# Performance work log

Measured on AMD Instinct MI355X. Metric: run time of the kernel, lower is better.

Reference implementation:

```python
import jax, jax.numpy as jnp
import numpy as np

THR = 1.0  # snntorch Leaky default threshold
BETA = 0.9


def setup_inputs() -> dict:
    key = jax.random.key(0)
    k_in, k_w1, k_b1, k_w2, k_b2 = jax.random.split(key, 5)
    T, B, D, H = 100, 256, 784, 256
    # binary spike train input (rate-coded)
    spike_input = (jax.random.uniform(k_in, (T, B, D)) < 0.5).astype(jnp.float32)
    # nn.Linear init: U(-1/sqrt(fan_in), 1/sqrt(fan_in))
    lim1 = 1.0 / np.sqrt(D)
    lim2 = 1.0 / np.sqrt(H)
    W1 = jax.random.uniform(k_w1, (H, D), minval=-lim1, maxval=lim1, dtype=jnp.float32)
    b1 = jax.random.uniform(k_b1, (H,), minval=-lim1, maxval=lim1, dtype=jnp.float32)
    W2 = jax.random.uniform(k_w2, (D, H), minval=-lim2, maxval=lim2, dtype=jnp.float32)
    b2 = jax.random.uniform(k_b2, (D,), minval=-lim2, maxval=lim2, dtype=jnp.float32)
    return {"spike_input": spike_input, "W1": W1, "b1": b1, "W2": W2, "b2": b2}


def _heaviside(x):
    return (x > 0).astype(x.dtype)


def reference(spike_input, W1, b1, W2, b2):
    T, B, D = spike_input.shape
    H = W1.shape[0]

    def step(carry, x_t):
        mem1, mem2 = carry
        # layer 1: Linear + Leaky LIF (reset-by-subtraction, as in snntorch)
        cur1 = x_t @ W1.T + b1                          # [B,H]
        reset1 = _heaviside(mem1 - THR)                 # spikes from previous mem
        mem1 = BETA * mem1 + cur1 - reset1 * THR
        spk1 = _heaviside(mem1 - THR)
        # layer 2
        cur2 = spk1 @ W2.T + b2                         # [B,D]
        reset2 = _heaviside(mem2 - THR)
        mem2 = BETA * mem2 + cur2 - reset2 * THR
        spk2 = _heaviside(mem2 - THR)
        return (mem1, mem2), spk2

    mem1_0 = jnp.zeros((B, H), dtype=spike_input.dtype)
    mem2_0 = jnp.zeros((B, D), dtype=spike_input.dtype)
    _, spk_out = jax.lax.scan(step, (mem1_0, mem2_0), spike_input)
    return spk_out  # [T,B,D]
```

## Files before the change

### kernel.cpp

```cpp
#include <hip/hip_runtime.h>

typedef __attribute__((ext_vector_type(8))) _Float16 f16x8;
typedef __attribute__((ext_vector_type(4))) float f32x4;

static constexpr int TT = 100, BB = 256, DD = 784, HH = 256;
static constexpr int MM = TT * BB;
static constexpr int K1PAD = 800;
static constexpr int DPAD = 832;
static constexpr float MIDSC = 2048.0f, INVMID = 1.0f / 2048.0f;

__device__ __forceinline__ unsigned short f2h(float x) {
  _Float16 h = (_Float16)x;
  return *(unsigned short*)&h;
}
__device__ __forceinline__ float h2f(unsigned short u) {
  _Float16 h = *(_Float16*)&u;
  return (float)h;
}
__device__ __forceinline__ void glds16(const void* g, void* l) {
  __builtin_amdgcn_global_load_lds(
      (const __attribute__((address_space(1))) unsigned int*)g,
      (__attribute__((address_space(3))) unsigned int*)l, 16, 0, 0);
}

__global__ __launch_bounds__(256)
void split_w(const float* __restrict__ W, unsigned short* __restrict__ Ws,
             int N, int K, int Npad, int Kpad) {
  int idx = blockIdx.x * 256 + threadIdx.x;
  int total = Npad * Kpad;
  if (idx >= total) return;
  int row = idx / Kpad, col = idx - row * Kpad;
  float w = (row < N && col < K) ? W[row * K + col] : 0.0f;
  unsigned short h0 = f2h(w);
  float r = (w - h2f(h0)) * MIDSC;
  Ws[idx] = h0;
  Ws[total + idx] = f2h(r);
}

__global__ __launch_bounds__(256, 2)
void gemm1(const float* __restrict__ X, const unsigned short* __restrict__ Bs,
           const float* __restrict__ bias, float* __restrict__ C) {
  constexpr int Kpad = K1PAD, nkb = Kpad / 32;
  __shared__ unsigned short Asm[2][128 * 32];
  __shared__ unsigned short Bsm[3][2][128 * 32];
  const int tid = threadIdx.x;
  const int bm = blockIdx.x * 128, bn = blockIdx.y * 128;
  const int wid = tid >> 6, lane = tid & 63;
  const int wr = (wid >> 1) * 64, wc = (wid & 1) * 64;
  const int l15 = lane & 15, l4 = lane >> 4;

  f32x4 acc[2][4][4];
#pragma unroll
  for (int s = 0; s < 2; ++s)
#pragma unroll
    for (int m = 0; m < 4; ++m)
#pragma unroll
      for (int n = 0; n < 4; ++n) acc[s][m][n] = (f32x4){0.f, 0.f, 0.f, 0.f};

  const int rl = wid * 32 + (lane >> 2);
  const int ce = ((lane & 3) ^ ((lane >> 3) & 3)) * 8;
  const size_t pstr = (size_t)HH * Kpad;
  const unsigned short* bsrc0 = Bs + (size_t)(bn + rl) * Kpad + ce;
  const unsigned short* bsrc1 = Bs + (size_t)(bn + rl + 16) * Kpad + ce;

  const int rdsw = (l4 ^ ((l15 >> 1) & 3)) * 8;

  const int r0 = tid >> 2;
  const int c0log = (tid & 3) * 8;
  const int c0phys = ((tid & 3) ^ ((tid >> 3) & 3)) * 8;

  float4 aA[4], aB[4];

  auto loadA = [&](int kb, float4 (&d)[4]) {
    const int col = kb * 32 + c0log;
    const bool ok = col < DD;
    const int colc = ok ? col : 0;
    const float* p0 = &X[(size_t)(bm + r0) * DD + colc];
    const float* p1 = &X[(size_t)(bm + r0 + 64) * DD + colc];
    d[0] = *(const float4*)p0; d[1] = *(const float4*)(p0 + 4);
    d[2] = *(const float4*)p1; d[3] = *(const float4*)(p1 + 4);
    if (!ok) {
      const float4 z = make_float4(0.f, 0.f, 0.f, 0.f);
      d[0] = z; d[1] = z; d[2] = z; d[3] = z;
    }
  };
  auto packA = [&](int bi, const float4 (&s_)[4]) {
    const unsigned ONE = 0x3C00u;
    auto pk = [&](float a, float b) {
      return (a != 0.f ? ONE : 0u) | (b != 0.f ? (ONE << 16) : 0u);
    };
    uint4 v0, v1;
    v0.x = pk(s_[0].x, s_[0].y); v0.y = pk(s_[0].z, s_[0].w);
    v0.z = pk(s_[1].x, s_[1].y); v0.w = pk(s_[1].z, s_[1].w);
    v1.x = pk(s_[2].x, s_[2].y); v1.y = pk(s_[2].z, s_[2].w);
    v1.z = pk(s_[3].x, s_[3].y); v1.w = pk(s_[3].z, s_[3].w);
    *(uint4*)&Asm[bi][r0 * 32 + c0phys] = v0;
    *(uint4*)&Asm[bi][(r0 + 64) * 32 + c0phys] = v1;
  };
  auto stageB = [&](int t) {
    const int k0 = t * 32, bi = t % 3;
    glds16(bsrc0 + k0, &Bsm[bi][0][(wid * 32) * 32]);
    glds16(bsrc1 + k0, &Bsm[bi][0][(wid * 32 + 16) * 32]);
    glds16(bsrc0 + pstr + k0, &Bsm[bi][1][(wid * 32) * 32]);
    glds16(bsrc1 + pstr + k0, &Bsm[bi][1][(wid * 32 + 16) * 32]);
  };
  auto compute = [&](int kb) {
    const int cb = kb & 1, b3 = kb % 3;
    f16x8 afr[4];
#pragma unroll
    for (int m = 0; m < 4; ++m)
      afr[m] = *(const f16x8*)&Asm[cb][(wr + m * 16 + l15) * 32 + rdsw];
#pragma unroll
    for (int s = 0; s < 2; ++s) {
      f16x8 bfr[4];
#pragma unroll
      for (int n = 0; n < 4; ++n)
        bfr[n] = *(const f16x8*)&Bsm[b3][s][(wc + n * 16 + l15) * 32 + rdsw];
#pragma unroll
      for (int m = 0; m < 4; ++m)
#pragma unroll
        for (int n = 0; n < 4; ++n)
          acc[s][m][n] = __builtin_amdgcn_mfma_f32_16x16x32_f16(afr[m], bfr[n], acc[s][m][n], 0, 0, 0);
    }
  };
  auto stepK = [&](int kb, const float4 (&pk_)[4], float4 (&ld_)[4]) {
    if (kb + 2 < nkb) stageB(kb + 2);
    compute(kb);
    __builtin_amdgcn_sched_barrier(0);
    if (kb + 2 < nkb) asm volatile("s_waitcnt vmcnt(4)" ::: "memory");
    else              asm volatile("s_waitcnt vmcnt(0)" ::: "memory");
    if (kb + 1 < nkb) packA((kb + 1) & 1, pk_);
    if (kb + 2 < nkb) loadA(kb + 2, ld_);
    asm volatile("s_waitcnt lgkmcnt(0)" ::: "memory");
    __builtin_amdgcn_sched_barrier(0);
    __builtin_amdgcn_s_barrier();
    __builtin_amdgcn_sched_barrier(0);
  };

  loadA(0, aA);
  stageB(0); stageB(1);
  asm volatile("s_waitcnt vmcnt(8)" ::: "memory");
  packA(0, aA);
  loadA(1, aB);
  asm volatile("s_waitcnt vmcnt(8)" ::: "memory");
  asm volatile("s_waitcnt lgkmcnt(0)" ::: "memory");
  __builtin_amdgcn_s_barrier();
  __builtin_amdgcn_sched_barrier(0);

  for (int kb2 = 0; kb2 < nkb; kb2 += 2) {
    stepK(kb2, aB, aA);
    if (kb2 + 1 < nkb) stepK(kb2 + 1, aA, aB);
  }

#pragma unroll
  for (int m = 0; m < 4; ++m)
#pragma unroll
    for (int n = 0; n < 4; ++n) {
      const int col = bn + wc + n * 16 + l15;
      const float bv = bias[col];
#pragma unroll
      for (int r = 0; r < 4; ++r) {
        const int row = bm + wr + m * 16 + l4 * 4 + r;
        C[(size_t)row * HH + col] = fmaf(acc[1][m][n][r], INVMID, acc[0][m][n][r]) + bv;
      }
    }
}

__global__ __launch_bounds__(256)
void lif_scan_h4(const float4* __restrict__ cur, uint2* __restrict__ spk,
                 int NE4, int nt) {
  const int tid = blockIdx.x * 256 + threadIdx.x;
  float4 mem = make_float4(0.f, 0.f, 0.f, 0.f);
  auto step1 = [](float& m, float c) {
    const float reset = (m > 1.0f) ? 1.0f : 0.0f;
    m = __fsub_rn(__fadd_rn(__fmul_rn(0.9f, m), c), reset);
    return (m > 1.0f);
  };
#pragma unroll 4
  for (int t = 0; t < nt; ++t) {
    const float4 c = cur[(size_t)t * NE4 + tid];
    unsigned s0 = step1(mem.x, c.x) ? 0x3C00u : 0u;
    unsigned s1 = step1(mem.y, c.y) ? 0x3C00u : 0u;
    unsigned s2 = step1(mem.z, c.z) ? 0x3C00u : 0u;
    unsigned s3 = step1(mem.w, c.w) ? 0x3C00u : 0u;
    uint2 o;
    o.x = s0 | (s1 << 16);
    o.y = s2 | (s3 << 16);
    spk[(size_t)t * NE4 + tid] = o;
  }
}

__global__ __launch_bounds__(256, 1)
void fused_l2(const unsigned short* __restrict__ spk1,
              const unsigned short* __restrict__ W2s,
              const float* __restrict__ b2, float* __restrict__ out) {
  __shared__ unsigned short Asm[3][16 * 256];
  const int tid = threadIdx.x, wid = tid >> 6, lane = tid & 63;
  const int l15 = lane & 15, l4 = lane >> 4;
  const int b0 = blockIdx.x * 16;
  const int d0 = blockIdx.y * 64;
  const int col = d0 + wid * 16 + l15;
  const bool st = (col < DD);

  f16x8 wfr[2][8];
#pragma unroll
  for (int s = 0; s < 2; ++s)
#pragma unroll
    for (int ks = 0; ks < 8; ++ks)
      wfr[s][ks] = *(const f16x8*)&W2s[(size_t)s * DPAD * HH + (size_t)col * HH + ks * 32 + l4 * 8];
  const float bv = st ? b2[col] : 0.f;

  const unsigned short* asrc[2];
#pragma unroll
  for (int i = 0; i < 2; ++i) {
    const int r = (wid * 2 + i) * 2 + (lane >> 5);
    const int e = ((lane & 31) * 8) ^ ((r & 7) << 3);
    asrc[i] = spk1 + (size_t)(b0 + r) * HH + e;
  }
  auto stageA = [&](int t) {
    const int bi = t % 3;
    const size_t toff = (size_t)t * (BB * HH);
    glds16(asrc[0] + toff, &Asm[bi][(wid * 2) * 512]);
    glds16(asrc[1] + toff, &Asm[bi][(wid * 2 + 1) * 512]);
  };

  f32x4 mem = (f32x4){0.f, 0.f, 0.f, 0.f};
  const size_t obase = (size_t)(b0 + l4 * 4) * DD + col;

  stageA(0); stageA(1);
  asm volatile("s_waitcnt vmcnt(2)" ::: "memory");
  __builtin_amdgcn_s_barrier();
  __builtin_amdgcn_sched_barrier(0);

  for (int t = 0; t < TT; ++t) {
    if (t + 2 < TT) stageA(t + 2);
    const int bi = t % 3;
    f32x4 a0 = (f32x4){0.f, 0.f, 0.f, 0.f};
    f32x4 a1 = (f32x4){0.f, 0.f, 0.f, 0.f};
#pragma unroll
    for (int ks = 0; ks < 8; ++ks) {
      const int ro = l15 * 256 + ((ks * 32 + l4 * 8) ^ ((l15 & 7) << 3));
      const f16x8 afr = *(const f16x8*)&Asm[bi][ro];
      a0 = __builtin_amdgcn_mfma_f32_16x16x32_f16(afr, wfr[0][ks], a0, 0, 0, 0);
      a1 = __builtin_amdgcn_mfma_f32_16x16x32_f16(afr, wfr[1][ks], a1, 0, 0, 0);
    }
    if (st) {
#pragma unroll
      for (int r = 0; r < 4; ++r) {
        const float cur = fmaf(a1[r], INVMID, a0[r]) + bv;
        const float reset = (mem[r] > 1.0f) ? 1.0f : 0.0f;
        mem[r] = __fsub_rn(__fadd_rn(__fmul_rn(0.9f, mem[r]), cur), reset);
        out[(size_t)t * (BB * DD) + obase + (size_t)r * DD] = (mem[r] > 1.0f) ? 1.0f : 0.0f;
      }
    }
    __builtin_amdgcn_sched_barrier(0);
    if (t + 2 < TT) {
      if (st) asm volatile("s_waitcnt vmcnt(6)" ::: "memory");
      else    asm volatile("s_waitcnt vmcnt(2)" ::: "memory");
    } else if (t + 1 < TT) {
      if (st) asm volatile("s_waitcnt vmcnt(4)" ::: "memory");
      else    asm volatile("s_waitcnt vmcnt(0)" ::: "memory");
    }
    if (t + 1 < TT) {
      __builtin_amdgcn_s_barrier();
      __builtin_amdgcn_sched_barrier(0);
    }
  }
}

extern "C" void kernel_launch(void* const* d_in, const int* in_sizes, int n_in,
                              void* d_out, int out_size, void* d_ws, size_t ws_size,
                              hipStream_t stream) {
  const float* x  = (const float*)d_in[0];
  const float* W1 = (const float*)d_in[1];
  const float* b1 = (const float*)d_in[2];
  const float* W2 = (const float*)d_in[3];
  const float* b2 = (const float*)d_in[4];
  float* out = (float*)d_out;

  const size_t w1s_elems = (size_t)2 * HH * K1PAD;
  const size_t w2s_elems = (size_t)2 * DPAD * HH;
  unsigned short* W1s = (unsigned short*)d_ws;
  unsigned short* W2s = W1s + w1s_elems;
  float* cur1 = (float*)(W2s + w2s_elems);
  unsigned short* spk1 = (unsigned short*)(cur1 + (size_t)MM * HH);

  dim3 blk(256);

  split_w<<<dim3((HH * K1PAD + 255) / 256), blk, 0, stream>>>(W1, W1s, HH, DD, HH, K1PAD);
  split_w<<<dim3((DPAD * HH + 255) / 256), blk, 0, stream>>>(W2, W2s, DD, HH, DPAD, HH);

  gemm1<<<dim3(MM / 128, HH / 128), blk, 0, stream>>>(x, W1s, b1, cur1);

  lif_scan_h4<<<dim3((BB * HH / 4) / 256), blk, 0, stream>>>(
      (const float4*)cur1, (uint2*)spk1, BB * HH / 4, TT);

  fused_l2<<<dim3(BB / 16, DPAD / 64), blk, 0, stream>>>(spk1, W2s, b2, out);
}
```

Measured before the change: 113.6 us.

## Drop LDS staging in layer-2 kernel; load spikes directly into registers per wave

The layer-2 fused kernel no longer stages spike tiles through shared memory with async global-to-LDS copies and block barriers. Each wave now owns an independent 16x16 output tile, indexed from a flattened 1-D grid, and loads its A fragments straight from global memory into registers, double-buffered across pairs of timesteps. The D padding to 832 is removed, so there are no idle padded columns and no bounds predicate. This removes barrier synchronisation and LDS traffic, but each wave re-reads spike rows that were previously shared across the block, and the manual waitcnt control is given up in favour of compiler scheduling.

```diff
diff --git a/kernel.cpp b/kernel.cpp
--- a/kernel.cpp
+++ b/kernel.cpp
@@ -6,7 +6,6 @@
 static constexpr int TT = 100, BB = 256, DD = 784, HH = 256;
 static constexpr int MM = TT * BB;
 static constexpr int K1PAD = 800;
-static constexpr int DPAD = 832;
 static constexpr float MIDSC = 2048.0f, INVMID = 1.0f / 2048.0f;
 
 __device__ __forceinline__ unsigned short f2h(float x) {
@@ -190,81 +189,66 @@
   }
 }
 
-__global__ __launch_bounds__(256, 1)
+__global__ __launch_bounds__(256)
 void fused_l2(const unsigned short* __restrict__ spk1,
               const unsigned short* __restrict__ W2s,
               const float* __restrict__ b2, float* __restrict__ out) {
-  __shared__ unsigned short Asm[3][16 * 256];
-  const int tid = threadIdx.x, wid = tid >> 6, lane = tid & 63;
+  const int gw = (blockIdx.x << 2) | (threadIdx.x >> 6);
+  const int lane = threadIdx.x & 63;
   const int l15 = lane & 15, l4 = lane >> 4;
-  const int b0 = blockIdx.x * 16;
-  const int d0 = blockIdx.y * 64;
-  const int col = d0 + wid * 16 + l15;
-  const bool st = (col < DD);
+  const int bb = gw / 49, dd = gw - bb * 49;
+  const int b0 = bb * 16, d0 = dd * 16;
 
   f16x8 wfr[2][8];
+  const unsigned short* wbase = W2s + (size_t)(d0 + l15) * HH + l4 * 8;
 #pragma unroll
   for (int s = 0; s < 2; ++s)
 #pragma unroll
     for (int ks = 0; ks < 8; ++ks)
-      wfr[s][ks] = *(const f16x8*)&W2s[(size_t)s * DPAD * HH + (size_t)col * HH + ks * 32 + l4 * 8];
-  const float bv = st ? b2[col] : 0.f;
-
-  const unsigned short* asrc[2];
-#pragma unroll
-  for (int i = 0; i < 2; ++i) {
-    const int r = (wid * 2 + i) * 2 + (lane >> 5);
-    const int e = ((lane & 31) * 8) ^ ((r & 7) << 3);
-    asrc[i] = spk1 + (size_t)(b0 + r) * HH + e;
-  }
-  auto stageA = [&](int t) {
-    const int bi = t % 3;
-    const size_t toff = (size_t)t * (BB * HH);
-    glds16(asrc[0] + toff, &Asm[bi][(wid * 2) * 512]);
-    glds16(asrc[1] + toff, &Asm[bi][(wid * 2 + 1) * 512]);
-  };
+      wfr[s][ks] = *(const f16x8*)(wbase + (size_t)s * ((size_t)DD * HH) + ks * 32);
+  const float bv = b2[d0 + l15];
+
+  const unsigned short* abase = spk1 + (size_t)(b0 + l15) * HH + l4 * 8;
+  float* obase = out + (size_t)(b0 + l4 * 4) * DD + d0 + l15;
 
   f32x4 mem = (f32x4){0.f, 0.f, 0.f, 0.f};
-  const size_t obase = (size_t)(b0 + l4 * 4) * DD + col;
-
-  stageA(0); stageA(1);
-  asm volatile("s_waitcnt vmcnt(2)" ::: "memory");
-  __builtin_amdgcn_s_barrier();
-  __builtin_amdgcn_sched_barrier(0);
-
-  for (int t = 0; t < TT; ++t) {
-    if (t + 2 < TT) stageA(t + 2);
-    const int bi = t % 3;
-    f32x4 a0 = (f32x4){0.f, 0.f, 0.f, 0.f};
-    f32x4 a1 = (f32x4){0.f, 0.f, 0.f, 0.f};
+  f16x8 aX[8], aY[8];
+
+#pragma unroll
+  for (int ks = 0; ks < 8; ++ks)
+    aX[ks] = *(const f16x8*)(abase + ks * 32);
+
+  auto body = [&](int t, const f16x8 (&a)[8]) {
+    f32x4 p0 = (f32x4){0.f, 0.f, 0.f, 0.f};
+    f32x4 p1 = (f32x4){0.f, 0.f, 0.f, 0.f};
 #pragma unroll
     for (int ks = 0; ks < 8; ++ks) {
-      const int ro = l15 * 256 + ((ks * 32 + l4 * 8) ^ ((l15 & 7) << 3));
-      const f16x8 afr = *(const f16x8*)&Asm[bi][ro];
-      a0 = __builtin_amdgcn_mfma_f32_16x16x32_f16(afr, wfr[0][ks], a0, 0, 0, 0);
-      a1 = __builtin_amdgcn_mfma_f32_16x16x32_f16(afr, wfr[1][ks], a1, 0, 0, 0);
-    }
-    if (st) {
-#pragma unroll
-      for (int r = 0; r < 4; ++r) {
-        const float cur = fmaf(a1[r], INVMID, a0[r]) + bv;
-        const float reset = (mem[r] > 1.0f) ? 1.0f : 0.0f;
-        mem[r] = __fsub_rn(__fadd_rn(__fmul_rn(0.9f, mem[r]), cur), reset);
-        out[(size_t)t * (BB * DD) + obase + (size_t)r * DD] = (mem[r] > 1.0f) ? 1.0f : 0.0f;
-      }
-    }
-    __builtin_amdgcn_sched_barrier(0);
+      p0 = __builtin_amdgcn_mfma_f32_16x16x32_f16(a[ks], wfr[0][ks], p0, 0, 0, 0);
+      p1 = __builtin_amdgcn_mfma_f32_16x16x32_f16(a[ks], wfr[1][ks], p1, 0, 0, 0);
+    }
+    float* op = obase + (size_t)t * ((size_t)BB * DD);
+#pragma unroll
+    for (int r = 0; r < 4; ++r) {
+      const float cur = fmaf(p1[r], INVMID, p0[r]) + bv;
+      const float reset = (mem[r] > 1.0f) ? 1.0f : 0.0f;
+      mem[r] = __fsub_rn(__fadd_rn(__fmul_rn(0.9f, mem[r]), cur), reset);
+      op[(size_t)r * DD] = (mem[r] > 1.0f) ? 1.0f : 0.0f;
+    }
+  };
+
+  for (int t = 0; t < TT; t += 2) {
+    const unsigned short* p1 = abase + (size_t)(t + 1) * (BB * HH);
+#pragma unroll
+    for (int ks = 0; ks < 8; ++ks)
+      aY[ks] = *(const f16x8*)(p1 + ks * 32);
+    body(t, aX);
     if (t + 2 < TT) {
-      if (st) asm volatile("s_waitcnt vmcnt(6)" ::: "memory");
-      else    asm volatile("s_waitcnt vmcnt(2)" ::: "memory");
-    } else if (t + 1 < TT) {
-      if (st) asm volatile("s_waitcnt vmcnt(4)" ::: "memory");
-      else    asm volatile("s_waitcnt vmcnt(0)" ::: "memory");
-    }
-    if (t + 1 < TT) {
-      __builtin_amdgcn_s_barrier();
-      __builtin_amdgcn_sched_barrier(0);
-    }
+      const unsigned short* p2 = abase + (size_t)(t + 2) * (BB * HH);
+#pragma unroll
+      for (int ks = 0; ks < 8; ++ks)
+        aX[ks] = *(const f16x8*)(p2 + ks * 32);
+    }
+    body(t + 1, aY);
   }
 }
 
@@ -279,7 +263,7 @@
   float* out = (float*)d_out;
 
   const size_t w1s_elems = (size_t)2 * HH * K1PAD;
-  const size_t w2s_elems = (size_t)2 * DPAD * HH;
+  const size_t w2s_elems = (size_t)2 * DD * HH;
   unsigned short* W1s = (unsigned short*)d_ws;
   unsigned short* W2s = W1s + w1s_elems;
   float* cur1 = (float*)(W2s + w2s_elems);
@@ -288,12 +272,12 @@
   dim3 blk(256);
 
   split_w<<<dim3((HH * K1PAD + 255) / 256), blk, 0, stream>>>(W1, W1s, HH, DD, HH, K1PAD);
-  split_w<<<dim3((DPAD * HH + 255) / 256), blk, 0, stream>>>(W2, W2s, DD, HH, DPAD, HH);
+  split_w<<<dim3((DD * HH + 255) / 256), blk, 0, stream>>>(W2, W2s, DD, HH, DD, HH);
 
   gemm1<<<dim3(MM / 128, HH / 128), blk, 0, stream>>>(x, W1s, b1, cur1);
 
   lif_scan_h4<<<dim3((BB * HH / 4) / 256), blk, 0, stream>>>(
       (const float4*)cur1, (uint2*)spk1, BB * HH / 4, TT);
 
-  fused_l2<<<dim3(BB / 16, DPAD / 64), blk, 0, stream>>>(spk1, W2s, b2, out);
-}
+  fused_l2<<<dim3(16 * 49 / 4), blk, 0, stream>>>(spk1, W2s, b2, out);
+}
```

Result: slower. 154.1 us (+35.7%).

## Shrink fused layer-2 blocks to two waves, trim D padding, reorder A packing

Applied to the files above, without the earlier changes.

The fused layer-2 kernel now runs 128-thread blocks that each cover 32 output columns, on a flattened 400-block grid instead of 16x13 blocks of 256 threads. D padding drops from 832 to 800, which removes wasted work on padded columns. Each wave now stages four rows of spikes per timestep, and the vmcnt waits are retuned to match. In gemm1, the A packing step moves ahead of B staging and compute, so its latency can overlap. The added risk is more redundant staging of spikes per output column and fragile hand-tuned waitcnt counts.

```diff
diff --git a/kernel.cpp b/kernel.cpp
--- a/kernel.cpp
+++ b/kernel.cpp
@@ -6,7 +6,7 @@
 static constexpr int TT = 100, BB = 256, DD = 784, HH = 256;
 static constexpr int MM = TT * BB;
 static constexpr int K1PAD = 800;
-static constexpr int DPAD = 832;
+static constexpr int N2PAD = 800;
 static constexpr float MIDSC = 2048.0f, INVMID = 1.0f / 2048.0f;
 
 __device__ __forceinline__ unsigned short f2h(float x) {
@@ -124,12 +124,12 @@
     }
   };
   auto stepK = [&](int kb, const float4 (&pk_)[4], float4 (&ld_)[4]) {
+    if (kb + 1 < nkb) packA((kb + 1) & 1, pk_);
     if (kb + 2 < nkb) stageB(kb + 2);
     compute(kb);
     __builtin_amdgcn_sched_barrier(0);
     if (kb + 2 < nkb) asm volatile("s_waitcnt vmcnt(4)" ::: "memory");
     else              asm volatile("s_waitcnt vmcnt(0)" ::: "memory");
-    if (kb + 1 < nkb) packA((kb + 1) & 1, pk_);
     if (kb + 2 < nkb) loadA(kb + 2, ld_);
     asm volatile("s_waitcnt lgkmcnt(0)" ::: "memory");
     __builtin_amdgcn_sched_barrier(0);
@@ -190,75 +190,81 @@
   }
 }
 
-__global__ __launch_bounds__(256, 1)
+__global__ __launch_bounds__(128)
 void fused_l2(const unsigned short* __restrict__ spk1,
               const unsigned short* __restrict__ W2s,
               const float* __restrict__ b2, float* __restrict__ out) {
   __shared__ unsigned short Asm[3][16 * 256];
   const int tid = threadIdx.x, wid = tid >> 6, lane = tid & 63;
   const int l15 = lane & 15, l4 = lane >> 4;
-  const int b0 = blockIdx.x * 16;
-  const int d0 = blockIdx.y * 64;
-  const int col = d0 + wid * 16 + l15;
-  const bool st = (col < DD);
+  const int bb = blockIdx.x / 25, dblk = blockIdx.x - bb * 25;
+  const int b0 = bb * 16;
+  const int d0 = dblk * 32 + wid * 16;
+  const bool st = (d0 < DD);
+  const int d0c = st ? d0 : 0;
 
   f16x8 wfr[2][8];
+  const unsigned short* wb = W2s + (size_t)(d0c + l15) * HH + l4 * 8;
 #pragma unroll
   for (int s = 0; s < 2; ++s)
 #pragma unroll
     for (int ks = 0; ks < 8; ++ks)
-      wfr[s][ks] = *(const f16x8*)&W2s[(size_t)s * DPAD * HH + (size_t)col * HH + ks * 32 + l4 * 8];
-  const float bv = st ? b2[col] : 0.f;
-
-  const unsigned short* asrc[2];
-#pragma unroll
-  for (int i = 0; i < 2; ++i) {
-    const int r = (wid * 2 + i) * 2 + (lane >> 5);
+      wfr[s][ks] = *(const f16x8*)(wb + (size_t)s * (N2PAD * HH) + ks * 32);
+  const float bv = st ? b2[d0 + l15] : 0.f;
+
+  const unsigned short* asrc[4];
+#pragma unroll
+  for (int i = 0; i < 4; ++i) {
+    const int r = wid * 8 + 2 * i + (lane >> 5);
     const int e = ((lane & 31) * 8) ^ ((r & 7) << 3);
     asrc[i] = spk1 + (size_t)(b0 + r) * HH + e;
   }
   auto stageA = [&](int t) {
     const int bi = t % 3;
     const size_t toff = (size_t)t * (BB * HH);
-    glds16(asrc[0] + toff, &Asm[bi][(wid * 2) * 512]);
-    glds16(asrc[1] + toff, &Asm[bi][(wid * 2 + 1) * 512]);
+#pragma unroll
+    for (int i = 0; i < 4; ++i)
+      glds16(asrc[i] + toff, &Asm[bi][(wid * 8 + 2 * i) * 256]);
   };
 
   f32x4 mem = (f32x4){0.f, 0.f, 0.f, 0.f};
-  const size_t obase = (size_t)(b0 + l4 * 4) * DD + col;
+  float* obase = out + (size_t)(b0 + l4 * 4) * DD + d0c + l15;
 
   stageA(0); stageA(1);
-  asm volatile("s_waitcnt vmcnt(2)" ::: "memory");
+  asm volatile("s_waitcnt vmcnt(4)" ::: "memory");
   __builtin_amdgcn_s_barrier();
   __builtin_amdgcn_sched_barrier(0);
 
   for (int t = 0; t < TT; ++t) {
     if (t + 2 < TT) stageA(t + 2);
     const int bi = t % 3;
-    f32x4 a0 = (f32x4){0.f, 0.f, 0.f, 0.f};
-    f32x4 a1 = (f32x4){0.f, 0.f, 0.f, 0.f};
+    f32x4 p0 = (f32x4){0.f, 0.f, 0.f, 0.f};
+    f32x4 p1 = (f32x4){0.f, 0.f, 0.f, 0.f};
 #pragma unroll
     for (int ks = 0; ks < 8; ++ks) {
-      const int ro = l15 * 256 + ((ks * 32 + l4 * 8) ^ ((l15 & 7) << 3));
-      const f16x8 afr = *(const f16x8*)&Asm[bi][ro];
-      a0 = __builtin_amdgcn_mfma_f32_16x16x32_f16(afr, wfr[0][ks], a0, 0, 0, 0);
-      a1 = __builtin_amdgcn_mfma_f32_16x16x32_f16(afr, wfr[1][ks], a1, 0, 0, 0);
+      const f16x8 a = *(const f16x8*)&Asm[bi][l15 * 256 + ((ks * 32 + l4 * 8) ^ ((l15 & 7) << 3))];
+      p0 = __builtin_amdgcn_mfma_f32_16x16x32_f16(a, wfr[0][ks], p0, 0, 0, 0);
+      p1 = __builtin_amdgcn_mfma_f32_16x16x32_f16(a, wfr[1][ks], p1, 0, 0, 0);
     }
     if (st) {
+      float* op = obase + (size_t)t * ((size_t)BB * DD);
 #pragma unroll
       for (int r = 0; r < 4; ++r) {
-        const float cur = fmaf(a1[r], INVMID, a0[r]) + bv;
+        const float cur = fmaf(p1[r], INVMID, p0[r]) + bv;
         const float reset = (mem[r] > 1.0f) ? 1.0f : 0.0f;
         mem[r] = __fsub_rn(__fadd_rn(__fmul_rn(0.9f, mem[r]), cur), reset);
-        out[(size_t)t * (BB * DD) + obase + (size_t)r * DD] = (mem[r] > 1.0f) ? 1.0f : 0.0f;
+        op[(size_t)r * DD] = (mem[r] > 1.0f) ? 1.0f : 0.0f;
       }
     }
     __builtin_amdgcn_sched_barrier(0);
-    if (t + 2 < TT) {
-      if (st) asm volatile("s_waitcnt vmcnt(6)" ::: "memory");
-      else    asm volatile("s_waitcnt vmcnt(2)" ::: "memory");
+    if (t == 0) {
+      if (st) asm volatile("s_waitcnt vmcnt(8)" ::: "memory");
+      else    asm volatile("s_waitcnt vmcnt(4)" ::: "memory");
+    } else if (t + 2 < TT) {
+      if (st) asm volatile("s_waitcnt vmcnt(12)" ::: "memory");
+      else    asm volatile("s_waitcnt vmcnt(4)" ::: "memory");
     } else if (t + 1 < TT) {
-      if (st) asm volatile("s_waitcnt vmcnt(4)" ::: "memory");
+      if (st) asm volatile("s_waitcnt vmcnt(8)" ::: "memory");
       else    asm volatile("s_waitcnt vmcnt(0)" ::: "memory");
     }
     if (t + 1 < TT) {
@@ -279,7 +285,7 @@
   float* out = (float*)d_out;
 
   const size_t w1s_elems = (size_t)2 * HH * K1PAD;
-  const size_t w2s_elems = (size_t)2 * DPAD * HH;
+  const size_t w2s_elems = (size_t)2 * N2PAD * HH;
   unsigned short* W1s = (unsigned short*)d_ws;
   unsigned short* W2s = W1s + w1s_elems;
   float* cur1 = (float*)(W2s + w2s_elems);
@@ -288,12 +294,12 @@
   dim3 blk(256);
 
   split_w<<<dim3((HH * K1PAD + 255) / 256), blk, 0, stream>>>(W1, W1s, HH, DD, HH, K1PAD);
-  split_w<<<dim3((DPAD * HH + 255) / 256), blk, 0, stream>>>(W2, W2s, DD, HH, DPAD, HH);
+  split_w<<<dim3((N2PAD * HH + 255) / 256), blk, 0, stream>>>(W2, W2s, DD, HH, N2PAD, HH);
 
   gemm1<<<dim3(MM / 128, HH / 128), blk, 0, stream>>>(x, W1s, b1, cur1);
 
   lif_scan_h4<<<dim3((BB * HH / 4) / 256), blk, 0, stream>>>(
       (const float4*)cur1, (uint2*)spk1, BB * HH / 4, TT);
 
-  fused_l2<<<dim3(BB / 16, DPAD / 64), blk, 0, stream>>>(spk1, W2s, b2, out);
-}
+  fused_l2<<<dim3(16 * 25), dim3(128), 0, stream>>>(spk1, W2s, b2, out);
+}
```

After: 120.3 us. +5.9%, slower.
